# Kernel tuning notes

Hardware: AMD Instinct MI355X
Metric: run time of the kernel (lower is better)

Reference implementation:

```python
import jax, jax.numpy as jnp
import numpy as np

BINS = 30
MOMENTUM = 0.75


def setup_inputs() -> dict:
    key = jax.random.key(0)
    k1, k2 = jax.random.split(key)
    B = 16777216
    x = jax.random.normal(k1, (B, 2), dtype=jnp.float32)
    target = jax.random.randint(k2, (B,), 0, 2, dtype=jnp.int32)
    return {"x": x, "target": target}


def reference(x, target):
    # GHM-C loss with binary one-hot labels built as [1 - t, t].
    B = x.shape[0]
    t = target.astype(x.dtype)
    labels = jnp.stack([1.0 - t, t], axis=-1)  # (B, 2)

    # gradient magnitude g = |p_true - 1| = |sum(softmax(x) * labels) - 1|, detached
    p = jax.nn.softmax(x, axis=-1)
    g = jnp.abs(jnp.sum(p * labels, axis=-1) - 1.0)  # (B,) in [0, 1]
    g = jax.lax.stop_gradient(g)

    # histogram binning: edges[i] = i/bins, last edge nudged by 1e-6 so g==1 lands in last bin
    bin_idx = jnp.clip((g * BINS).astype(jnp.int32), 0, BINS - 1)  # (B,)
    counts = jax.ops.segment_sum(jnp.ones_like(g), bin_idx, num_segments=BINS)  # (BINS,)

    # EMA of bin counts; acc_sum starts at zero so first step is (1 - momentum) * count
    acc = (1.0 - MOMENTUM) * counts
    nonzero = counts > 0
    n = jnp.sum(nonzero.astype(x.dtype))

    beta_per_bin = jnp.where(nonzero, jnp.asarray(B, x.dtype) / jnp.where(nonzero, acc, 1.0), 0.0)
    beta = beta_per_bin[bin_idx] / jnp.maximum(n, 1.0)  # (B,)
    beta = jax.lax.stop_gradient(beta)

    # weighted soft-label cross entropy
    ce = -jnp.sum(jax.nn.log_softmax(x, axis=-1) * labels, axis=-1)  # (B,)
    return jnp.mean(beta * ce)
```

## Files before the change

kernel.cpp:

```cpp
#include <hip/hip_runtime.h>

#define NBINS 30
#define NREP  8
#define SSCALE 512.0f
#define CNT_SHIFT 22
#define SUM_MASK ((1u << CNT_SHIFT) - 1)

typedef float f32x4 __attribute__((ext_vector_type(4)));
typedef int   i32x4 __attribute__((ext_vector_type(4)));


__device__ __forceinline__ void ghm_one(float x0, float x1, int t,
                                        unsigned int* __restrict__ h) {
    float nz  = (t != 0) ? (x0 - x1) : (x1 - x0);
    float em  = __expf(-fabsf(nz));
    float inv = __builtin_amdgcn_rcpf(1.0f + em);
    float ce  = fmaxf(nz, 0.0f) + __logf(1.0f + em);
    float g   = (nz >= 0.0f) ? inv : (1.0f - inv);

    int bin = (int)(g * 30.0f);
    bin = bin > NBINS - 1 ? NBINS - 1 : bin;

    unsigned int v = (1u << CNT_SHIFT) + (unsigned int)(ce * SSCALE + 0.5f);
    atomicAdd(&h[bin], v);
}

__device__ __forceinline__ void ghm4(f32x4 xa, f32x4 xb, i32x4 tv,
                                     unsigned int* __restrict__ h) {
    ghm_one(xa.x, xa.y, tv.x, h);
    ghm_one(xa.z, xa.w, tv.y, h);
    ghm_one(xb.x, xb.y, tv.z, h);
    ghm_one(xb.z, xb.w, tv.w, h);
}

__global__ __launch_bounds__(256) void ghm_pass1(const f32x4* __restrict__ x,
                                                 const i32x4* __restrict__ tgt,
                                                 unsigned int* __restrict__ gcnt,
                                                 unsigned long long* __restrict__ gsum,
                                                 int ngroups) {
    __shared__ unsigned int hist[16][33];

    for (int i = threadIdx.x; i < 16 * 33; i += 256)
        ((unsigned int*)hist)[i] = 0u;
    __syncthreads();

    unsigned int* h = hist[threadIdx.x >> 4];

    const int stride = gridDim.x * blockDim.x;
    const int tid    = blockIdx.x * blockDim.x + threadIdx.x;
    const int iters  = ngroups / stride;

    if (iters > 0) {
        int   i  = tid;
        f32x4 xa = __builtin_nontemporal_load(&x[2 * i]);
        f32x4 xb = __builtin_nontemporal_load(&x[2 * i + 1]);
        i32x4 tv = __builtin_nontemporal_load(&tgt[i]);
        for (int it = 1; it < iters; ++it) {
            const int j = i + stride;
            f32x4 nxa = __builtin_nontemporal_load(&x[2 * j]);
            f32x4 nxb = __builtin_nontemporal_load(&x[2 * j + 1]);
            i32x4 ntv = __builtin_nontemporal_load(&tgt[j]);
            ghm4(xa, xb, tv, h);
            xa = nxa; xb = nxb; tv = ntv; i = j;
        }
        ghm4(xa, xb, tv, h);
    }
    {
        const int j = tid + iters * stride;
        if (j < ngroups) {
            f32x4 xa = __builtin_nontemporal_load(&x[2 * j]);
            f32x4 xb = __builtin_nontemporal_load(&x[2 * j + 1]);
            i32x4 tv = __builtin_nontemporal_load(&tgt[j]);
            ghm4(xa, xb, tv, h);
        }
    }
    __syncthreads();

    if (threadIdx.x < NBINS) {
        int b = threadIdx.x;
        unsigned int       c = 0u;
        unsigned long long s = 0ull;
        #pragma unroll
        for (int q = 0; q < 16; ++q) {
            unsigned int v = hist[q][b];
            c += v >> CNT_SHIFT;
            s += v & SUM_MASK;
        }
        if (c) {
            int rep = blockIdx.x & (NREP - 1);
            atomicAdd(&gcnt[rep * 32 + b], c);
            atomicAdd(&gsum[rep * 32 + b], s);
        }
    }
}

__global__ void ghm_finalize(const unsigned int* __restrict__ gcnt,
                             const unsigned long long* __restrict__ gsum,
                             float* __restrict__ out) {
    int b = threadIdx.x;
    double term = 0.0;
    int    nzb  = 0;
    if (b < NBINS) {
        unsigned long long c = 0ull, s = 0ull;
        #pragma unroll
        for (int r = 0; r < NREP; ++r) {
            c += gcnt[r * 32 + b];
            s += gsum[r * 32 + b];
        }
        if (c) { nzb = 1; term = ((double)s * (1.0 / 512.0)) / (double)c; }
    }
    #pragma unroll
    for (int m = 16; m >= 1; m >>= 1) {
        term += __shfl_xor(term, m, 32);
        nzb  += __shfl_xor(nzb,  m, 32);
    }
    if (threadIdx.x == 0)
        out[0] = (float)((nzb > 0) ? 4.0 * term / (double)nzb : 0.0);
}

extern "C" void kernel_launch(void* const* d_in, const int* in_sizes, int n_in,
                              void* d_out, int out_size, void* d_ws, size_t ws_size,
                              hipStream_t stream) {
    const f32x4* x   = (const f32x4*)d_in[0];
    const i32x4* tgt = (const i32x4*)d_in[1];
    const int B = in_sizes[1];
    const int ngroups = B / 4;

    unsigned int*       gcnt = (unsigned int*)d_ws;
    unsigned long long* gsum = (unsigned long long*)((char*)d_ws + 1024);

    (void)hipMemsetAsync(d_ws, 0, 3072, stream);

    ghm_pass1<<<2048, 256, 0, stream>>>(x, tgt, gcnt, gsum, ngroups);
    ghm_finalize<<<1, 64, 0, stream>>>(gcnt, gsum, (float*)d_out);
}
```

Baseline: 44.09 us.

## Replace global atomics and memset with per-block partials reduced in finalize

Each block now writes its per-bin count and sum partials to its own slot in workspace instead of atomically adding into 8 replicated global counters. This removes the memset launch and global atomic contention. The finalize kernel grows to 1024 threads and reduces 2048 partials through LDS atomics. The shared histogram copies also double from 16 to 32, so 8 threads share each copy instead of 16, cutting LDS atomic contention in the main loop at the cost of a slightly longer block-level merge.

```diff
diff --git a/kernel.cpp b/kernel.cpp
--- a/kernel.cpp
+++ b/kernel.cpp
@@ -1,7 +1,7 @@
 #include <hip/hip_runtime.h>
 
 #define NBINS 30
-#define NREP  8
+#define NBLK  2048
 #define SSCALE 512.0f
 #define CNT_SHIFT 22
 #define SUM_MASK ((1u << CNT_SHIFT) - 1)
@@ -35,16 +35,16 @@
 
 __global__ __launch_bounds__(256) void ghm_pass1(const f32x4* __restrict__ x,
                                                  const i32x4* __restrict__ tgt,
-                                                 unsigned int* __restrict__ gcnt,
-                                                 unsigned long long* __restrict__ gsum,
+                                                 unsigned int* __restrict__ cnt,
+                                                 unsigned long long* __restrict__ sum,
                                                  int ngroups) {
-    __shared__ unsigned int hist[16][33];
+    __shared__ unsigned int hist[32][33];
 
-    for (int i = threadIdx.x; i < 16 * 33; i += 256)
+    for (int i = threadIdx.x; i < 32 * 33; i += 256)
         ((unsigned int*)hist)[i] = 0u;
     __syncthreads();
 
-    unsigned int* h = hist[threadIdx.x >> 4];
+    unsigned int* h = hist[threadIdx.x >> 3];
 
     const int stride = gridDim.x * blockDim.x;
     const int tid    = blockIdx.x * blockDim.x + threadIdx.x;
@@ -76,46 +76,59 @@
     }
     __syncthreads();
 
-    if (threadIdx.x < NBINS) {
+    if (threadIdx.x < 32) {
         int b = threadIdx.x;
         unsigned int       c = 0u;
         unsigned long long s = 0ull;
         #pragma unroll
-        for (int q = 0; q < 16; ++q) {
+        for (int q = 0; q < 32; ++q) {
             unsigned int v = hist[q][b];
             c += v >> CNT_SHIFT;
             s += v & SUM_MASK;
         }
-        if (c) {
-            int rep = blockIdx.x & (NREP - 1);
-            atomicAdd(&gcnt[rep * 32 + b], c);
-            atomicAdd(&gsum[rep * 32 + b], s);
-        }
+        cnt[blockIdx.x * 32 + b] = c;
+        sum[blockIdx.x * 32 + b] = s;
     }
 }
 
-__global__ void ghm_finalize(const unsigned int* __restrict__ gcnt,
-                             const unsigned long long* __restrict__ gsum,
-                             float* __restrict__ out) {
-    int b = threadIdx.x;
-    double term = 0.0;
-    int    nzb  = 0;
-    if (b < NBINS) {
-        unsigned long long c = 0ull, s = 0ull;
+__global__ __launch_bounds__(1024) void ghm_finalize(
+        const unsigned int* __restrict__ cnt,
+        const unsigned long long* __restrict__ sum,
+        float* __restrict__ out, int nblocks) {
+    __shared__ unsigned long long lds_c[32];
+    __shared__ unsigned long long lds_s[32];
+
+    const int bin   = threadIdx.x & 31;
+    const int chunk = threadIdx.x >> 5;
+
+    if (threadIdx.x < 32) { lds_c[threadIdx.x] = 0ull; lds_s[threadIdx.x] = 0ull; }
+    __syncthreads();
+
+    unsigned long long c = 0ull, s = 0ull;
+    for (int i = chunk; i < nblocks; i += 32) {
+        c += cnt[i * 32 + bin];
+        s += sum[i * 32 + bin];
+    }
+    atomicAdd(&lds_c[bin], c);
+    atomicAdd(&lds_s[bin], s);
+    __syncthreads();
+
+    if (threadIdx.x < 32) {
+        int b = threadIdx.x;
+        double term = 0.0;
+        int    nzb  = 0;
+        if (b < NBINS) {
+            unsigned long long cb = lds_c[b];
+            if (cb) { nzb = 1; term = ((double)lds_s[b] * (1.0 / 512.0)) / (double)cb; }
+        }
         #pragma unroll
-        for (int r = 0; r < NREP; ++r) {
-            c += gcnt[r * 32 + b];
-            s += gsum[r * 32 + b];
+        for (int m = 16; m >= 1; m >>= 1) {
+            term += __shfl_xor(term, m, 32);
+            nzb  += __shfl_xor(nzb,  m, 32);
         }
-        if (c) { nzb = 1; term = ((double)s * (1.0 / 512.0)) / (double)c; }
+        if (b == 0)
+            out[0] = (float)((nzb > 0) ? 4.0 * term / (double)nzb : 0.0);
     }
-    #pragma unroll
-    for (int m = 16; m >= 1; m >>= 1) {
-        term += __shfl_xor(term, m, 32);
-        nzb  += __shfl_xor(nzb,  m, 32);
-    }
-    if (threadIdx.x == 0)
-        out[0] = (float)((nzb > 0) ? 4.0 * term / (double)nzb : 0.0);
 }
 
 extern "C" void kernel_launch(void* const* d_in, const int* in_sizes, int n_in,
@@ -126,11 +139,9 @@
     const int B = in_sizes[1];
     const int ngroups = B / 4;
 
-    unsigned int*       gcnt = (unsigned int*)d_ws;
-    unsigned long long* gsum = (unsigned long long*)((char*)d_ws + 1024);
+    unsigned int*       cnt = (unsigned int*)d_ws;
+    unsigned long long* sum = (unsigned long long*)((char*)d_ws + NBLK * 32 * 4);
 
-    (void)hipMemsetAsync(d_ws, 0, 3072, stream);
-
-    ghm_pass1<<<2048, 256, 0, stream>>>(x, tgt, gcnt, gsum, ngroups);
-    ghm_finalize<<<1, 64, 0, stream>>>(gcnt, gsum, (float*)d_out);
+    ghm_pass1<<<NBLK, 256, 0, stream>>>(x, tgt, cnt, sum, ngroups);
+    ghm_finalize<<<1, 1024, 0, stream>>>(cnt, sum, (float*)d_out, NBLK);
 }
```

New measurement: 56.63 us. 28.4% more time.
